# Kernel tuning notes

Hardware: AMD Instinct MI355X
Metric: run time of the kernel (lower is better)

The kernel has to match this reference:

```python
import jax, jax.numpy as jnp
import numpy as np
from jax import lax

B, N, C = 8, 4096, 64
RATIO = 0.25
M = int(N * RATIO)          # sampled centers per cloud (fps ratio)
K = 64                      # max_num_neighbors in ball query
R = 0.2                     # ball_query_radius
H = 128                     # MLP width
NEG = jnp.float32(-1e30)


def setup_inputs() -> dict:
    key = jax.random.key(0)
    k1, k2, k3, k4 = jax.random.split(key, 4)
    x = jax.random.normal(k1, (B, N, C), jnp.float32)
    pos = jax.random.uniform(k2, (B, N, 3), jnp.float32)  # unit cube coords
    W1 = jax.random.normal(k3, (C + 3, H), jnp.float32) * 0.05
    b1 = jnp.zeros((H,), jnp.float32)
    W2 = jax.random.normal(k4, (H, H), jnp.float32) * 0.05
    b2 = jnp.zeros((H,), jnp.float32)
    return {"x": x, "pos": pos, "W1": W1, "b1": b1, "W2": W2, "b2": b2}


def _fps(pos):
    """Farthest point sampling on one cloud [N,3] -> M int32 indices (start at 0)."""
    d0 = jnp.sum((pos - pos[0]) ** 2, axis=-1)  # min sq-dist to selected set
    def step(mind, _):
        nxt = jnp.argmax(mind).astype(jnp.int32)
        d = jnp.sum((pos - pos[nxt]) ** 2, axis=-1)
        return jnp.minimum(mind, d), nxt
    _, idxs = lax.scan(step, d0, None, length=M - 1)
    return jnp.concatenate([jnp.zeros((1,), jnp.int32), idxs])


def reference(x, pos, W1, b1, W2, b2):
    # --- FPS sampling (per cloud, deterministic start) ---
    idx = jax.vmap(_fps)(pos)                      # [B,M]
    bidx = jnp.arange(B)[:, None]
    centers = pos[bidx, idx]                        # [B,M,3]

    # --- ball query: first K points within radius R of each center ---
    d2 = jnp.sum((centers[:, :, None, :] - pos[:, None, :, :]) ** 2, axis=-1)  # [B,M,N]
    in_ball = d2 <= R * R
    # prefer lowest index (torch_cluster radius returns up to K arbitrary/first hits)
    score = jnp.where(in_ball, -jnp.arange(N, dtype=jnp.float32), NEG)
    vals, nbr = lax.top_k(score, K)                 # nbr: [B,M,K] neighbor indices
    valid = vals > NEG / 2                          # [B,M,K]; center itself always valid

    # --- PointNetConv: gather -> local MLP on [x_j, pos_j - pos_i] -> max aggr ---
    b3 = jnp.arange(B)[:, None, None]
    xj = x[b3, nbr]                                  # [B,M,K,C]
    rel = pos[b3, nbr] - centers[:, :, None, :]      # [B,M,K,3]
    feat = jnp.concatenate([xj, rel], axis=-1)       # [B,M,K,C+3]
    h = jax.nn.relu(feat @ W1 + b1)
    h = jax.nn.relu(h @ W2 + b2)                     # [B,M,K,H]
    h = jnp.where(valid[..., None], h, NEG)
    out = jnp.max(h, axis=2)                          # [B,M,H] max aggregation
    return out, centers
```

## Files before the change

### kernel.cpp

```cpp
#include <hip/hip_runtime.h>

#define BN 8
#define NN 4096
#define CC 64
#define MM 1024
#define KK 64
#define HH 128

typedef __attribute__((ext_vector_type(8))) short short8;
typedef __attribute__((ext_vector_type(4))) float f32x4;
typedef unsigned long long u64;
typedef unsigned int u32;

__device__ inline unsigned short f2bf(float f) {
  union { float f; unsigned u; } v; v.f = f;
  unsigned r = v.u + 0x7FFFu + ((v.u >> 16) & 1u);
  return (unsigned short)(r >> 16);
}

__device__ inline float sqd(float ax, float ay, float az, float bx, float by, float bz) {
  float dx = __fsub_rn(ax, bx), dy = __fsub_rn(ay, by), dz = __fsub_rn(az, bz);
  return __fadd_rn(__fadd_rn(__fmul_rn(dx, dx), __fmul_rn(dy, dy)), __fmul_rn(dz, dz));
}

__global__ void prep_w(const float* __restrict__ W1, const float* __restrict__ W2,
                       short* __restrict__ W1T, short* __restrict__ W2T) {
  int t = blockIdx.x * 256 + threadIdx.x;
  if (t < 128 * 104) {
    int n = t / 104, k = t % 104;
    float v = (k < 67) ? W1[k * 128 + n] : 0.f;
    W1T[t] = (short)f2bf(v);
  }
  if (t < 128 * 136) {
    int n = t / 136, k = t % 136;
    float v = (k < 128) ? W2[k * 128 + n] : 0.f;
    W2T[t] = (short)f2bf(v);
  }
}

template <int CTRL, int RM>
__device__ __forceinline__ u64 dpp_mv(u64 k) {
  int lo = __builtin_amdgcn_update_dpp(0, (int)(u32)k, CTRL, RM, 0xF, false);
  int hi = __builtin_amdgcn_update_dpp(0, (int)(u32)(k >> 32), CTRL, RM, 0xF, false);
  return ((u64)(u32)hi << 32) | (u32)lo;
}

__device__ __forceinline__ u64 wave_kmax(u64 k) {
  u64 m;
  m = dpp_mv<0xB1, 0xF>(k); if (m > k) k = m;
  m = dpp_mv<0x4E, 0xF>(k); if (m > k) k = m;
  m = dpp_mv<0x141, 0xF>(k); if (m > k) k = m;
  m = dpp_mv<0x140, 0xF>(k); if (m > k) k = m;
  m = dpp_mv<0x142, 0xA>(k); if (m > k) k = m;
  m = dpp_mv<0x143, 0xC>(k); if (m > k) k = m;
  u32 lo = (u32)__builtin_amdgcn_readlane((int)(u32)k, 63);
  u32 hi = (u32)__builtin_amdgcn_readlane((int)(u32)(k >> 32), 63);
  return ((u64)hi << 32) | lo;
}

__global__ __launch_bounds__(256) void fps_k(const float* __restrict__ pos,
                                             float* __restrict__ centers) {
  const int b = blockIdx.x;
  const int tid = threadIdx.x;
  const int lane = tid & 63;
  const int wv = tid >> 6;
  __shared__ f32x4 sp4[NN];
  __shared__ u64 sk[2][4];

  const float* P = pos + (size_t)b * NN * 3;

  float px[16], py[16], pz[16], mind[16];
  u32 klo[16];
#pragma unroll
  for (int i = 0; i < 16; ++i) {
    int p = tid + i * 256;
    px[i] = P[p * 3 + 0];
    py[i] = P[p * 3 + 1];
    pz[i] = P[p * 3 + 2];
    klo[i] = ~(u32)p;
    f32x4 v; v[0] = px[i]; v[1] = py[i]; v[2] = pz[i]; v[3] = 0.f;
    sp4[p] = v;
  }
#pragma unroll
  for (int i = 0; i < 16; ++i)
    asm volatile("" : "+v"(px[i]), "+v"(py[i]), "+v"(pz[i]));

  const float c0x = P[0], c0y = P[1], c0z = P[2];
#pragma unroll
  for (int i = 0; i < 16; ++i) mind[i] = sqd(px[i], py[i], pz[i], c0x, c0y, c0z);

  if (tid == 0) {
    centers[(size_t)(b * MM) * 3 + 0] = c0x;
    centers[(size_t)(b * MM) * 3 + 1] = c0y;
    centers[(size_t)(b * MM) * 3 + 2] = c0z;
  }
  __syncthreads();

  for (int m = 1; m < MM; ++m) {
    u64 k[16];
#pragma unroll
    for (int i = 0; i < 16; ++i)
      k[i] = ((u64)__float_as_uint(mind[i]) << 32) | klo[i];
#pragma unroll
    for (int s = 8; s; s >>= 1)
#pragma unroll
      for (int i = 0; i < s; ++i)
        if (k[i + s] > k[i]) k[i] = k[i + s];

    u64 kw = wave_kmax(k[0]);
    if (lane == 0) sk[m & 1][wv] = kw;
    __syncthreads();
    u64 kb = sk[m & 1][0];
#pragma unroll
    for (int w = 1; w < 4; ++w) {
      u64 o = sk[m & 1][w];
      if (o > kb) kb = o;
    }
    const u32 bp = ~(u32)kb;
    const f32x4 c4 = sp4[bp];
    if (tid == 0) {
      centers[(size_t)(b * MM + m) * 3 + 0] = c4[0];
      centers[(size_t)(b * MM + m) * 3 + 1] = c4[1];
      centers[(size_t)(b * MM + m) * 3 + 2] = c4[2];
    }
#pragma unroll
    for (int i = 0; i < 16; ++i) {
      float d2 = sqd(px[i], py[i], pz[i], c4[0], c4[1], c4[2]);
      mind[i] = fminf(mind[i], d2);
    }
  }
}

__global__ __launch_bounds__(256) void sa_k(const float* __restrict__ x,
                                            const float* __restrict__ pos,
                                            const float* __restrict__ b1,
                                            const float* __restrict__ b2,
                                            const short* __restrict__ W1T,
                                            const short* __restrict__ W2T,
                                            const float* __restrict__ centers,
                                            float* __restrict__ out) {
  const int cm = blockIdx.x;
  const int b = cm >> 10;
  const int tid = threadIdx.x;
  const int lane = tid & 63, wv = tid >> 6;
  const int l15 = lane & 15, lg = lane >> 4;

  __shared__ short s_feat[64][104];
  __shared__ short s_h1[64][136];
  __shared__ int s_nbr[64];
  __shared__ int s_wcnt[4];

  const int n0 = wv * 32;
  short8 w1f[2][3], w2f[2][4];
#pragma unroll
  for (int nt = 0; nt < 2; ++nt) {
    int row = n0 + nt * 16 + l15;
#pragma unroll
    for (int kt = 0; kt < 3; ++kt)
      w1f[nt][kt] = *reinterpret_cast<const short8*>(W1T + row * 104 + kt * 32 + lg * 8);
#pragma unroll
    for (int kt = 0; kt < 4; ++kt)
      w2f[nt][kt] = *reinterpret_cast<const short8*>(W2T + row * 136 + kt * 32 + lg * 8);
  }

  const float* Pb = pos + (size_t)b * NN * 3;
  const float cx = centers[(size_t)cm * 3 + 0];
  const float cy = centers[(size_t)cm * 3 + 1];
  const float cz = centers[(size_t)cm * 3 + 2];

  int cnt = 0;
  for (int base = 0; base < NN; base += 256) {
    int p = base + tid;
    float d2 = sqd(Pb[p * 3 + 0], Pb[p * 3 + 1], Pb[p * 3 + 2], cx, cy, cz);
    bool pred = d2 <= 0.04f;
    unsigned long long mask = __ballot(pred);
    if (lane == 0) s_wcnt[wv] = __popcll(mask);
    __syncthreads();
    int wbase = cnt, tot = 0;
#pragma unroll
    for (int w = 0; w < 4; ++w) {
      int c = s_wcnt[w];
      tot += c;
      if (w < wv) wbase += c;
    }
    if (pred) {
      int slot = wbase + (int)__popcll(mask & ((1ull << lane) - 1ull));
      if (slot < KK) s_nbr[slot] = p;
    }
    cnt += tot;
    __syncthreads();
    if (cnt >= KK) break;
  }
  if (cnt > KK) cnt = KK;

  {
    int* fz = (int*)&s_feat[0][0];
    for (int i = tid; i < 64 * 104 / 2; i += 256) fz[i] = 0;
  }
  __syncthreads();

  {
    const int j = tid >> 2, q = tid & 3;
    if (j < cnt) {
      int nj = s_nbr[j];
      const float* xr = x + ((size_t)b * NN + nj) * CC + q * 16;
      unsigned* dst = (unsigned*)&s_feat[j][q * 16];
#pragma unroll
      for (int v4 = 0; v4 < 4; ++v4) {
        f32x4 xv = *reinterpret_cast<const f32x4*>(xr + v4 * 4);
        unsigned lo0 = (unsigned)f2bf(xv[0]) | ((unsigned)f2bf(xv[1]) << 16);
        unsigned lo1 = (unsigned)f2bf(xv[2]) | ((unsigned)f2bf(xv[3]) << 16);
        dst[v4 * 2 + 0] = lo0;
        dst[v4 * 2 + 1] = lo1;
      }
      if (q == 0) {
        s_feat[j][64] = (short)f2bf(__fsub_rn(Pb[nj * 3 + 0], cx));
        s_feat[j][65] = (short)f2bf(__fsub_rn(Pb[nj * 3 + 1], cy));
        s_feat[j][66] = (short)f2bf(__fsub_rn(Pb[nj * 3 + 2], cz));
      }
    }
  }
  __syncthreads();

  f32x4 acc[4][2];
#pragma unroll
  for (int mt = 0; mt < 4; ++mt)
#pragma unroll
    for (int nt = 0; nt < 2; ++nt) acc[mt][nt] = (f32x4)0.f;

#pragma unroll
  for (int mt = 0; mt < 4; ++mt) {
    int arow = mt * 16 + l15;
#pragma unroll
    for (int kt = 0; kt < 3; ++kt) {
      short8 af = *reinterpret_cast<const short8*>(&s_feat[arow][kt * 32 + lg * 8]);
      acc[mt][0] = __builtin_amdgcn_mfma_f32_16x16x32_bf16(af, w1f[0][kt], acc[mt][0], 0, 0, 0);
      acc[mt][1] = __builtin_amdgcn_mfma_f32_16x16x32_bf16(af, w1f[1][kt], acc[mt][1], 0, 0, 0);
    }
  }

#pragma unroll
  for (int mt = 0; mt < 4; ++mt) {
#pragma unroll
    for (int nt = 0; nt < 2; ++nt) {
      int col = n0 + nt * 16 + l15;
      float bias = b1[col];
#pragma unroll
      for (int r = 0; r < 4; ++r) {
        int row = mt * 16 + lg * 4 + r;
        float h = fmaxf(__fadd_rn(acc[mt][nt][r], bias), 0.f);
        s_h1[row][col] = (short)f2bf(h);
      }
    }
  }
  __syncthreads();

  f32x4 acc2[4][2];
#pragma unroll
  for (int mt = 0; mt < 4; ++mt)
#pragma unroll
    for (int nt = 0; nt < 2; ++nt) acc2[mt][nt] = (f32x4)0.f;

#pragma unroll
  for (int mt = 0; mt < 4; ++mt) {
    int arow = mt * 16 + l15;
#pragma unroll
    for (int kt = 0; kt < 4; ++kt) {
      short8 af = *reinterpret_cast<const short8*>(&s_h1[arow][kt * 32 + lg * 8]);
      acc2[mt][0] = __builtin_amdgcn_mfma_f32_16x16x32_bf16(af, w2f[0][kt], acc2[mt][0], 0, 0, 0);
      acc2[mt][1] = __builtin_amdgcn_mfma_f32_16x16x32_bf16(af, w2f[1][kt], acc2[mt][1], 0, 0, 0);
    }
  }

#pragma unroll
  for (int nt = 0; nt < 2; ++nt) {
    int col = n0 + nt * 16 + l15;
    float bias = b2[col];
    float mx = -1e30f;
#pragma unroll
    for (int mt = 0; mt < 4; ++mt) {
#pragma unroll
      for (int r = 0; r < 4; ++r) {
        int row = mt * 16 + lg * 4 + r;
        float h = fmaxf(__fadd_rn(acc2[mt][nt][r], bias), 0.f);
        if (row < cnt) mx = fmaxf(mx, h);
      }
    }
    mx = fmaxf(mx, __shfl_xor(mx, 16));
    mx = fmaxf(mx, __shfl_xor(mx, 32));
    if (lg == 0) out[(size_t)cm * HH + col] = mx;
  }
}

extern "C" void kernel_launch(void* const* d_in, const int* in_sizes, int n_in,
                              void* d_out, int out_size, void* d_ws, size_t ws_size,
                              hipStream_t stream) {
  const float* x = (const float*)d_in[0];
  const float* pos = (const float*)d_in[1];
  const float* W1 = (const float*)d_in[2];
  const float* b1 = (const float*)d_in[3];
  const float* W2 = (const float*)d_in[4];
  const float* b2 = (const float*)d_in[5];

  float* out = (float*)d_out;
  float* centers = out + (size_t)BN * MM * HH;

  char* ws = (char*)d_ws;
  short* W1T = (short*)ws;
  short* W2T = (short*)(ws + 26624);

  prep_w<<<68, 256, 0, stream>>>(W1, W2, W1T, W2T);
  fps_k<<<BN, 256, 0, stream>>>(pos, centers);
  sa_k<<<BN * MM, 256, 0, stream>>>(x, pos, b1, b2, W1T, W2T, centers, out);
}
```

Before: 758.6 us.

## Restructure FPS argmax with float-only wave max, packed math, 512 threads

The farthest point sampling kernel now runs 512 threads with 8 contiguous points each and holds coordinates in float2 vectors, so distance updates can use packed FP32 ops. The 64-bit key argmax is replaced by a float-only DPP wave max followed by a second pass in which matching threads atomicMin their lowest index into shared memory. This cuts per-iteration reduction work on the serial critical path, in exchange for an extra barrier and a shared atomic each iteration. Tie-breaking still picks the lowest index, as before.

```diff
diff --git a/kernel.cpp b/kernel.cpp
--- a/kernel.cpp
+++ b/kernel.cpp
@@ -9,6 +9,7 @@
 
 typedef __attribute__((ext_vector_type(8))) short short8;
 typedef __attribute__((ext_vector_type(4))) float f32x4;
+typedef __attribute__((ext_vector_type(2))) float f32x2;
 typedef unsigned long long u64;
 typedef unsigned int u32;
 
@@ -39,94 +40,112 @@
 }
 
 template <int CTRL, int RM>
-__device__ __forceinline__ u64 dpp_mv(u64 k) {
-  int lo = __builtin_amdgcn_update_dpp(0, (int)(u32)k, CTRL, RM, 0xF, false);
-  int hi = __builtin_amdgcn_update_dpp(0, (int)(u32)(k >> 32), CTRL, RM, 0xF, false);
-  return ((u64)(u32)hi << 32) | (u32)lo;
-}
-
-__device__ __forceinline__ u64 wave_kmax(u64 k) {
-  u64 m;
-  m = dpp_mv<0xB1, 0xF>(k); if (m > k) k = m;
-  m = dpp_mv<0x4E, 0xF>(k); if (m > k) k = m;
-  m = dpp_mv<0x141, 0xF>(k); if (m > k) k = m;
-  m = dpp_mv<0x140, 0xF>(k); if (m > k) k = m;
-  m = dpp_mv<0x142, 0xA>(k); if (m > k) k = m;
-  m = dpp_mv<0x143, 0xC>(k); if (m > k) k = m;
-  u32 lo = (u32)__builtin_amdgcn_readlane((int)(u32)k, 63);
-  u32 hi = (u32)__builtin_amdgcn_readlane((int)(u32)(k >> 32), 63);
-  return ((u64)hi << 32) | lo;
-}
-
-__global__ __launch_bounds__(256) void fps_k(const float* __restrict__ pos,
+__device__ __forceinline__ float dppf(float x) {
+  int v = __builtin_amdgcn_update_dpp(0, __float_as_int(x), CTRL, RM, 0xF, false);
+  return __int_as_float(v);
+}
+
+__device__ __forceinline__ float wave_fmax(float x) {
+  x = fmaxf(x, dppf<0xB1, 0xF>(x));
+  x = fmaxf(x, dppf<0x4E, 0xF>(x));
+  x = fmaxf(x, dppf<0x141, 0xF>(x));
+  x = fmaxf(x, dppf<0x140, 0xF>(x));
+  x = fmaxf(x, dppf<0x142, 0xA>(x));
+  x = fmaxf(x, dppf<0x143, 0xC>(x));
+  return __int_as_float(__builtin_amdgcn_readlane(__float_as_int(x), 63));
+}
+
+__global__ __launch_bounds__(512) void fps_k(const float* __restrict__ pos,
                                              float* __restrict__ centers) {
   const int b = blockIdx.x;
   const int tid = threadIdx.x;
   const int lane = tid & 63;
   const int wv = tid >> 6;
   __shared__ f32x4 sp4[NN];
-  __shared__ u64 sk[2][4];
+  __shared__ f32x4 svm4[2];
+  __shared__ u32 sminp[2];
 
   const float* P = pos + (size_t)b * NN * 3;
 
-  float px[16], py[16], pz[16], mind[16];
-  u32 klo[16];
-#pragma unroll
-  for (int i = 0; i < 16; ++i) {
-    int p = tid + i * 256;
-    px[i] = P[p * 3 + 0];
-    py[i] = P[p * 3 + 1];
-    pz[i] = P[p * 3 + 2];
-    klo[i] = ~(u32)p;
-    f32x4 v; v[0] = px[i]; v[1] = py[i]; v[2] = pz[i]; v[3] = 0.f;
-    sp4[p] = v;
-  }
-#pragma unroll
-  for (int i = 0; i < 16; ++i)
-    asm volatile("" : "+v"(px[i]), "+v"(py[i]), "+v"(pz[i]));
+  f32x2 X[4], Y[4], Z[4], M[4];
+#pragma unroll
+  for (int j = 0; j < 4; ++j) {
+    int p0 = tid * 8 + j * 2;
+    float x0 = P[p0 * 3 + 0], y0 = P[p0 * 3 + 1], z0 = P[p0 * 3 + 2];
+    float x1 = P[p0 * 3 + 3], y1 = P[p0 * 3 + 4], z1 = P[p0 * 3 + 5];
+    X[j].x = x0; X[j].y = x1;
+    Y[j].x = y0; Y[j].y = y1;
+    Z[j].x = z0; Z[j].y = z1;
+    f32x4 v0; v0[0] = x0; v0[1] = y0; v0[2] = z0; v0[3] = 0.f;
+    f32x4 v1; v1[0] = x1; v1[1] = y1; v1[2] = z1; v1[3] = 0.f;
+    sp4[p0] = v0;
+    sp4[p0 + 1] = v1;
+  }
+#pragma unroll
+  for (int j = 0; j < 4; ++j)
+    asm volatile("" : "+v"(X[j]), "+v"(Y[j]), "+v"(Z[j]));
 
   const float c0x = P[0], c0y = P[1], c0z = P[2];
-#pragma unroll
-  for (int i = 0; i < 16; ++i) mind[i] = sqd(px[i], py[i], pz[i], c0x, c0y, c0z);
+  {
+#pragma clang fp contract(off)
+    f32x2 cx; cx.x = c0x; cx.y = c0x;
+    f32x2 cy; cy.x = c0y; cy.y = c0y;
+    f32x2 cz; cz.x = c0z; cz.y = c0z;
+#pragma unroll
+    for (int j = 0; j < 4; ++j) {
+      f32x2 dx = X[j] - cx, dy = Y[j] - cy, dz = Z[j] - cz;
+      M[j] = (dx * dx + dy * dy) + dz * dz;
+    }
+  }
 
   if (tid == 0) {
     centers[(size_t)(b * MM) * 3 + 0] = c0x;
     centers[(size_t)(b * MM) * 3 + 1] = c0y;
     centers[(size_t)(b * MM) * 3 + 2] = c0z;
+    sminp[0] = 0xFFFFFFFFu;
+    sminp[1] = 0xFFFFFFFFu;
   }
   __syncthreads();
 
   for (int m = 1; m < MM; ++m) {
-    u64 k[16];
-#pragma unroll
-    for (int i = 0; i < 16; ++i)
-      k[i] = ((u64)__float_as_uint(mind[i]) << 32) | klo[i];
-#pragma unroll
-    for (int s = 8; s; s >>= 1)
-#pragma unroll
-      for (int i = 0; i < s; ++i)
-        if (k[i + s] > k[i]) k[i] = k[i + s];
-
-    u64 kw = wave_kmax(k[0]);
-    if (lane == 0) sk[m & 1][wv] = kw;
+    float mv = fmaxf(fmaxf(fmaxf(M[0].x, M[0].y), fmaxf(M[1].x, M[1].y)),
+                     fmaxf(fmaxf(M[2].x, M[2].y), fmaxf(M[3].x, M[3].y)));
+    float wmax = wave_fmax(mv);
+    if (lane == 0) ((float*)svm4)[wv] = wmax;
     __syncthreads();
-    u64 kb = sk[m & 1][0];
-#pragma unroll
-    for (int w = 1; w < 4; ++w) {
-      u64 o = sk[m & 1][w];
-      if (o > kb) kb = o;
-    }
-    const u32 bp = ~(u32)kb;
+    f32x4 s0 = svm4[0], s1 = svm4[1];
+    float bmax = fmaxf(fmaxf(fmaxf(s0[0], s0[1]), fmaxf(s0[2], s0[3])),
+                       fmaxf(fmaxf(s1[0], s1[1]), fmaxf(s1[2], s1[3])));
+    if (mv == bmax) {
+      u32 em = 0;
+#pragma unroll
+      for (int j = 0; j < 4; ++j) {
+        if (M[j].x == bmax) em |= 1u << (2 * j);
+        if (M[j].y == bmax) em |= 1u << (2 * j + 1);
+      }
+      atomicMin(&sminp[m & 1], (u32)(tid * 8 + (int)__builtin_ctz(em)));
+    }
+    if (tid == 0) sminp[(m + 1) & 1] = 0xFFFFFFFFu;
+    __syncthreads();
+    const u32 bp = sminp[m & 1];
     const f32x4 c4 = sp4[bp];
     if (tid == 0) {
       centers[(size_t)(b * MM + m) * 3 + 0] = c4[0];
       centers[(size_t)(b * MM + m) * 3 + 1] = c4[1];
       centers[(size_t)(b * MM + m) * 3 + 2] = c4[2];
     }
-#pragma unroll
-    for (int i = 0; i < 16; ++i) {
-      float d2 = sqd(px[i], py[i], pz[i], c4[0], c4[1], c4[2]);
-      mind[i] = fminf(mind[i], d2);
+    {
+#pragma clang fp contract(off)
+      f32x2 cx; cx.x = c4[0]; cx.y = c4[0];
+      f32x2 cy; cy.x = c4[1]; cy.y = c4[1];
+      f32x2 cz; cz.x = c4[2]; cz.y = c4[2];
+#pragma unroll
+      for (int j = 0; j < 4; ++j) {
+        f32x2 dx = X[j] - cx, dy = Y[j] - cy, dz = Z[j] - cz;
+        f32x2 d2 = (dx * dx + dy * dy) + dz * dz;
+        M[j].x = fminf(M[j].x, d2.x);
+        M[j].y = fminf(M[j].y, d2.y);
+      }
     }
   }
 }
@@ -310,6 +329,6 @@
   short* W2T = (short*)(ws + 26624);
 
   prep_w<<<68, 256, 0, stream>>>(W1, W2, W1T, W2T);
-  fps_k<<<BN, 256, 0, stream>>>(pos, centers);
+  fps_k<<<BN, 512, 0, stream>>>(pos, centers);
   sa_k<<<BN * MM, 256, 0, stream>>>(x, pos, b1, b2, W1T, W2T, centers, out);
 }
```

Result: slower. 834.1 us (+9.9%).
